# Performance work log

Measured on AMD Instinct MI355X. Metric: run time of the kernel, lower is better.

## Reference

```python
import jax, jax.numpy as jnp
import numpy as np

HEADS, POINTS = 8, 4
EPS = 1e-5
BS, C, H, W = 2, 256, 200, 200


def _layernorm(x, g, b):
    m = x.mean(-1, keepdims=True)
    v = ((x - m) ** 2).mean(-1, keepdims=True)
    return (x - m) / jnp.sqrt(v + EPS) * g + b


def _sine_pos(bs, Hh, Ww, num_feats, temperature=10000.0):
    # mmdet SinePositionalEncoding with all-zeros mask: cumsum of ones -> 1..H / 1..W
    y = jnp.arange(1, Hh + 1, dtype=jnp.float32)
    x = jnp.arange(1, Ww + 1, dtype=jnp.float32)
    dim_t = jnp.arange(num_feats, dtype=jnp.float32)
    dim_t = temperature ** (2.0 * jnp.floor(dim_t / 2.0) / num_feats)

    def interleave(p):  # p: [N, num_feats] -> [sin(p0),cos(p1),sin(p2),...]
        return jnp.stack((jnp.sin(p[:, 0::2]), jnp.cos(p[:, 1::2])), axis=-1).reshape(p.shape[0], -1)

    pos_x = interleave(x[:, None] / dim_t)  # [W, nf]
    pos_y = interleave(y[:, None] / dim_t)  # [H, nf]
    pos = jnp.concatenate([
        jnp.broadcast_to(pos_y[:, None, :], (Hh, Ww, num_feats)),
        jnp.broadcast_to(pos_x[None, :, :], (Hh, Ww, num_feats)),
    ], axis=-1)  # [H, W, 2*nf] (channel order matches cat((pos_y,pos_x),dim=1) after flatten/permute)
    return jnp.broadcast_to(pos.reshape(1, Hh * Ww, 2 * num_feats), (bs, Hh * Ww, 2 * num_feats))


def _bilinear_sample(v, x, y):
    # v: [bs, heads, H, W, hd]; x, y: [bs, heads, N] pixel coords (align_corners=False, zero padding)
    bs, nh, Hh, Ww, hd = v.shape
    vf = v.reshape(bs, nh, Hh * Ww, hd)
    x0 = jnp.floor(x)
    y0 = jnp.floor(y)
    wx = x - x0
    wy = y - y0

    def gather(xi, yi):
        valid = (xi >= 0) & (xi < Ww) & (yi >= 0) & (yi < Hh)
        xc = jnp.clip(xi, 0, Ww - 1).astype(jnp.int32)
        yc = jnp.clip(yi, 0, Hh - 1).astype(jnp.int32)
        idx = yc * Ww + xc
        g = jnp.take_along_axis(vf, idx[..., None], axis=2)  # [bs, nh, N, hd]
        return g * valid[..., None].astype(v.dtype)

    out = gather(x0, y0) * ((1 - wx) * (1 - wy))[..., None]
    out = out + gather(x0 + 1, y0) * (wx * (1 - wy))[..., None]
    out = out + gather(x0, y0 + 1) * ((1 - wx) * wy)[..., None]
    out = out + gather(x0 + 1, y0 + 1) * (wx * wy)[..., None]
    return out


def _dfa_layer(out, ref, pos, Hh, Ww, p):
    bs, Lq, Cc = out.shape
    hd = Cc // HEADS
    q = out + pos
    value = out @ p['vp_w'].T + p['vp_b']  # [bs, Lq, C]
    off = (q @ p['off_w'].T + p['off_b']).reshape(bs, Lq, HEADS, POINTS, 2)
    aw = jax.nn.softmax((q @ p['aw_w'].T + p['aw_b']).reshape(bs, Lq, HEADS, POINTS), axis=-1)
    norm = jnp.array([Ww, Hh], dtype=out.dtype)
    loc = ref[None, :, None, None, :] + off / norm  # [bs, Lq, heads, P, 2] normalized [0,1]
    x = loc[..., 0] * Ww - 0.5
    y = loc[..., 1] * Hh - 0.5
    v = value.reshape(bs, Lq, HEADS, hd).transpose(0, 2, 1, 3).reshape(bs, HEADS, Hh, Ww, hd)
    xt = x.transpose(0, 2, 1, 3).reshape(bs, HEADS, Lq * POINTS)
    yt = y.transpose(0, 2, 1, 3).reshape(bs, HEADS, Lq * POINTS)
    samp = _bilinear_sample(v, xt, yt).reshape(bs, HEADS, Lq, POINTS, hd)
    attn = jnp.einsum('bhqpd,bqhp->bqhd', samp, aw).reshape(bs, Lq, Cc)
    attn = attn @ p['op_w'].T + p['op_b']
    out = _layernorm(out + attn, p['ln1_g'], p['ln1_b'])
    ffn = jax.nn.relu(out @ p['l1_w'].T + p['l1_b']) @ p['l2_w'].T + p['l2_b']
    return _layernorm(out + ffn, p['ln2_g'], p['ln2_b'])


def setup_inputs() -> dict:
    key = jax.random.key(0)
    ks = jax.random.split(key, 20)
    s = 0.02
    L = 3
    return {
        'bev_feat': jax.random.normal(ks[0], (BS, C, H, W), jnp.float32),
        'proj_q_w': jax.random.normal(ks[1], (C, C), jnp.float32) * s,
        'proj_q_b': jax.random.normal(ks[2], (C,), jnp.float32) * s,
        'off_w': jax.random.normal(ks[3], (L, HEADS * POINTS * 2, C), jnp.float32) * s,
        'off_b': jax.random.normal(ks[4], (L, HEADS * POINTS * 2), jnp.float32) * s,
        'aw_w': jax.random.normal(ks[5], (L, HEADS * POINTS, C), jnp.float32) * s,
        'aw_b': jax.random.normal(ks[6], (L, HEADS * POINTS), jnp.float32) * s,
        'vp_w': jax.random.normal(ks[7], (L, C, C), jnp.float32) * s,
        'vp_b': jax.random.normal(ks[8], (L, C), jnp.float32) * s,
        'op_w': jax.random.normal(ks[9], (L, C, C), jnp.float32) * s,
        'op_b': jax.random.normal(ks[10], (L, C), jnp.float32) * s,
        'ln1_g': jnp.ones((L, C), jnp.float32),
        'ln1_b': jnp.zeros((L, C), jnp.float32),
        'l1_w': jax.random.normal(ks[11], (L, C, C), jnp.float32) * s,
        'l1_b': jax.random.normal(ks[12], (L, C), jnp.float32) * s,
        'l2_w': jax.random.normal(ks[13], (L, C, C), jnp.float32) * s,
        'l2_b': jax.random.normal(ks[14], (L, C), jnp.float32) * s,
        'ln2_g': jnp.ones((L, C), jnp.float32),
        'ln2_b': jnp.zeros((L, C), jnp.float32),
    }


def reference(bev_feat, proj_q_w, proj_q_b, off_w, off_b, aw_w, aw_b, vp_w, vp_b,
              op_w, op_b, ln1_g, ln1_b, l1_w, l1_b, l2_w, l2_b, ln2_g, ln2_b):
    bs, Cc, Hh, Ww = bev_feat.shape
    x = bev_feat.reshape(bs, Cc, Hh * Ww).transpose(0, 2, 1)  # [bs, HW, C]
    out = x @ proj_q_w.T + proj_q_b
    # reference points: pixel centers normalized to [0,1]
    ry, rx = jnp.meshgrid(jnp.linspace(0.5, Hh - 0.5, Hh) / Hh,
                          jnp.linspace(0.5, Ww - 0.5, Ww) / Ww, indexing='ij')
    ref = jnp.stack([rx.reshape(-1), ry.reshape(-1)], axis=-1).astype(bev_feat.dtype)  # [HW, 2]
    pos = _sine_pos(bs, Hh, Ww, Cc // 2).astype(bev_feat.dtype)
    n_layers = off_w.shape[0]
    for i in range(n_layers):
        p = dict(off_w=off_w[i], off_b=off_b[i], aw_w=aw_w[i], aw_b=aw_b[i],
                 vp_w=vp_w[i], vp_b=vp_b[i], op_w=op_w[i], op_b=op_b[i],
                 ln1_g=ln1_g[i], ln1_b=ln1_b[i], l1_w=l1_w[i], l1_b=l1_b[i],
                 l2_w=l2_w[i], l2_b=l2_b[i], ln2_g=ln2_g[i], ln2_b=ln2_b[i])
        out = _dfa_layer(out, ref, pos, Hh, Ww, p)
    return out.transpose(0, 2, 1).reshape(bs, Cc, Hh, Ww)
```

## Files before the change

kernel.cpp:

```cpp
#include <hip/hip_runtime.h>
#include <math.h>

#define HEADS 8
#define POINTS 4
#define BSZ 2
#define CDIM 256
#define HH 200
#define WW 200
#define LQ (HH * WW)
#define MTOT (BSZ * LQ)
#define NLAYERS 3
#define MPAD 40064

typedef __attribute__((ext_vector_type(8))) short shortx8;
typedef __attribute__((ext_vector_type(4))) float floatx4;

__device__ __forceinline__ ushort f2b(float f) {
    union { float f; unsigned u; } v; v.f = f;
    unsigned r = v.u + 0x7fffu + ((v.u >> 16) & 1u);
    return (ushort)(r >> 16);
}
__device__ __forceinline__ float b2f(ushort b) {
    union { unsigned u; float f; } v; v.u = ((unsigned)b) << 16;
    return v.f;
}
__device__ __forceinline__ float bitsf(unsigned u) {
    union { unsigned u; float f; } v; v.u = u;
    return v.f;
}
__device__ __forceinline__ uint packbf(float lo, float hi) {
    return (uint)f2b(lo) | ((uint)f2b(hi) << 16);
}

__device__ __forceinline__ int permc(int c) {
    return (c & ~63) | (((c & 15) << 2) | ((c & 63) >> 4));
}
__device__ __forceinline__ int iperm(int p) {
    return (p & ~63) | (((p & 3) << 4) | ((p & 63) >> 2));
}

__global__ __launch_bounds__(256)
void cvt_kernel(const float* __restrict__ in, ushort* __restrict__ out)
{
    const int i = (blockIdx.x * 256 + threadIdx.x) * 4;
    const float4 v = *(const float4*)(in + i);
    ushort4 o;
    o.x = f2b(v.x); o.y = f2b(v.y); o.z = f2b(v.z); o.w = f2b(v.w);
    *(ushort4*)(out + i) = o;
}

__global__ __launch_bounds__(256)
void cvt_perm_kernel(const float* __restrict__ in, ushort* __restrict__ out)
{
    const int idx = (blockIdx.x * 256 + threadIdx.x) * 4;
    const int rowb = idx & ~255;
    const int p0 = idx & 255;
    ushort4 o;
    o.x = f2b(in[rowb + iperm(p0 + 0)]);
    o.y = f2b(in[rowb + iperm(p0 + 1)]);
    o.z = f2b(in[rowb + iperm(p0 + 2)]);
    o.w = f2b(in[rowb + iperm(p0 + 3)]);
    *(ushort4*)(out + idx) = o;
}

__global__ __launch_bounds__(256)
void build_offaw(const float* __restrict__ offw, const float* __restrict__ offb,
                 const float* __restrict__ aww, const float* __restrict__ awb,
                 ushort* __restrict__ wout, float* __restrict__ bout)
{
    const int blk = blockIdx.x;
    const int i = blk >> 7;
    const int r = blk & 127;
    const int c = threadIdx.x;
    float v = 0.f;
    if (r < 64)      v = offw[((size_t)i * 64 + r) * CDIM + c];
    else if (r < 96) v = aww[((size_t)i * 32 + (r - 64)) * CDIM + c];
    wout[((size_t)i * 128 + r) * CDIM + permc(c)] = f2b(v);
    if (c == 0) {
        float bb = 0.f;
        if (r < 64)      bb = offb[i * 64 + r];
        else if (r < 96) bb = awb[i * 32 + (r - 64)];
        bout[i * 128 + r] = bb;
    }
}

__global__ __launch_bounds__(256)
void pos_kernel(ushort* __restrict__ pos)
{
    const int idx = blockIdx.x * 256 + threadIdx.x;
    const int c = idx & 255;
    const int l = idx >> 8;
    const int cc = c & 127;
    const float coord = (c < 128) ? (float)(l / WW + 1) : (float)(l % WW + 1);
    const float expo = (float)(2 * (cc >> 1)) * (1.0f / 128.0f);
    const float t = powf(10000.0f, expo);
    const float ph = coord / t;
    pos[(size_t)l * CDIM + permc(c)] = f2b((cc & 1) ? cosf(ph) : sinf(ph));
}

__global__ __launch_bounds__(256)
void bevT_kernel(const float* __restrict__ in, ushort* __restrict__ out)
{
    __shared__ float tile[32][33];
    const int b = blockIdx.z;
    const int l0 = blockIdx.x * 32;
    const int c0 = blockIdx.y * 32;
    const float* ib = in + (size_t)b * CDIM * LQ;
    ushort* ob = out + (size_t)b * LQ * CDIM;
    #pragma unroll
    for (int j = 0; j < 32; j += 8)
        tile[threadIdx.y + j][threadIdx.x] =
            ib[(size_t)(c0 + threadIdx.y + j) * LQ + l0 + threadIdx.x];
    __syncthreads();
    #pragma unroll
    for (int j = 0; j < 32; j += 8)
        ob[(size_t)(l0 + threadIdx.y + j) * CDIM + c0 + threadIdx.x] =
            f2b(tile[threadIdx.x][threadIdx.y + j]);
}

#define LSTR 40

template<bool RELU, bool F32OUT, bool BF16OUT, bool ROWADD>
__global__ __launch_bounds__(256)
void mfma_gemm(const ushort* __restrict__ A, const ushort* __restrict__ B,
               const float* __restrict__ bias,
               float* __restrict__ Cf, ushort* __restrict__ Cb,
               const ushort* __restrict__ rowtab,
               int N, int K)
{
    __shared__ ushort As[128 * LSTR];
    __shared__ ushort Bs[128 * LSTR];
    const int tid = threadIdx.x;
    const int lane = tid & 63;
    const int wave = tid >> 6;
    const int wr = (wave >> 1) * 64;
    const int wc = (wave & 1) * 64;
    const int rowBase = blockIdx.y * 128;
    const int colBase = blockIdx.x * 128;

    floatx4 acc[4][4];
    #pragma unroll
    for (int i = 0; i < 4; i++)
        #pragma unroll
        for (int j = 0; j < 4; j++) {
            floatx4 z = {0.f, 0.f, 0.f, 0.f};
            acc[i][j] = z;
        }

    const int strow = tid >> 2;
    const int stcol = (tid & 3) * 8;
    const int kq = (lane >> 4) * 8;
    const int lr = lane & 15;

    for (int k0 = 0; k0 < K; k0 += 32) {
        #pragma unroll
        for (int j = 0; j < 2; j++) {
            const int r = j * 64 + strow;
            const uint4 av = *(const uint4*)(A + (size_t)(rowBase + r) * K + k0 + stcol);
            const uint4 bv = *(const uint4*)(B + (size_t)(colBase + r) * K + k0 + stcol);
            *(uint4*)(As + r * LSTR + stcol) = av;
            *(uint4*)(Bs + r * LSTR + stcol) = bv;
        }
        __syncthreads();
        shortx8 af[4], bfr[4];
        #pragma unroll
        for (int t = 0; t < 4; t++) {
            af[t]  = *(const shortx8*)(As + (wr + t * 16 + lr) * LSTR + kq);
            bfr[t] = *(const shortx8*)(Bs + (wc + t * 16 + lr) * LSTR + kq);
        }
        #pragma unroll
        for (int mt = 0; mt < 4; mt++)
            #pragma unroll
            for (int nt = 0; nt < 4; nt++)
                acc[mt][nt] = __builtin_amdgcn_mfma_f32_16x16x32_bf16(
                    af[mt], bfr[nt], acc[mt][nt], 0, 0, 0);
        __syncthreads();
    }

    const int colB = colBase + wc + lr;
    const int rowB = rowBase + wr + (lane >> 4) * 4;
    #pragma unroll
    for (int mt = 0; mt < 4; mt++) {
        #pragma unroll
        for (int r = 0; r < 4; r++) {
            const int m = rowB + mt * 16 + r;
            const int pr = (m >= LQ) ? m - LQ : m;
            #pragma unroll
            for (int nt = 0; nt < 4; nt++) {
                const int n = colB + nt * 16;
                float v = acc[mt][nt][r];
                if (ROWADD) v += b2f(rowtab[(size_t)pr * 384 + n]);
                else        v += bias[n];
                if (RELU) v = fmaxf(v, 0.f);
                if (F32OUT) Cf[(size_t)m * N + n] = v;
                if (BF16OUT) Cb[(size_t)m * N + n] = f2b(v);
            }
        }
    }
}

template<bool RELU, bool LN, bool F32OUT, bool BF16OUT, bool PERMC>
__global__ __launch_bounds__(512, 1)
void gemm_fused(const ushort* __restrict__ A, const ushort* __restrict__ B,
                const float* __restrict__ bias,
                float* __restrict__ resid, ushort* __restrict__ Cb,
                const float* __restrict__ g, const float* __restrict__ beta)
{
    __shared__ ushort As[2][128 * LSTR];
    __shared__ ushort Bs[2][256 * LSTR];

    const int tid = threadIdx.x;
    const int lane = tid & 63;
    const int wave = tid >> 6;
    const int lr = lane & 15;
    const int hi = lane >> 4;
    const int rowBase = blockIdx.x * 128;
    const int wr = (wave >> 2) * 64;
    const int wc = (wave & 3) * 64;

    floatx4 acc[4][4];
    #pragma unroll
    for (int i = 0; i < 4; i++)
        #pragma unroll
        for (int j = 0; j < 4; j++) {
            floatx4 z = {0.f, 0.f, 0.f, 0.f};
            acc[i][j] = z;
        }

    const int strow = tid >> 2;
    const int stcol = (tid & 3) * 8;
    const int kq = hi * 8;

    const ushort* ag = A + (size_t)(rowBase + strow) * CDIM + stcol;
    const ushort* bg = B + (size_t)strow * CDIM + stcol;

    {
        const uint4 av  = *(const uint4*)(ag);
        const uint4 bv0 = *(const uint4*)(bg);
        const uint4 bv1 = *(const uint4*)(bg + 128 * CDIM);
        *(uint4*)(As[0] + strow * LSTR + stcol) = av;
        *(uint4*)(Bs[0] + strow * LSTR + stcol) = bv0;
        *(uint4*)(Bs[0] + (strow + 128) * LSTR + stcol) = bv1;
    }

    #pragma unroll
    for (int kt = 0; kt < 8; ++kt) {
        const int p = kt & 1;
        __syncthreads();
        uint4 av, bv0, bv1;
        if (kt < 7) {
            const int ko = (kt + 1) * 32;
            av  = *(const uint4*)(ag + ko);
            bv0 = *(const uint4*)(bg + ko);
            bv1 = *(const uint4*)(bg + ko + 128 * CDIM);
        }
        shortx8 af[4], bfr[4];
        #pragma unroll
        for (int t = 0; t < 4; t++) {
            af[t]  = *(const shortx8*)(As[p] + (wr + t * 16 + lr) * LSTR + kq);
            bfr[t] = *(const shortx8*)(Bs[p] + (wc + t * 16 + lr) * LSTR + kq);
        }
        #pragma unroll
        for (int mt = 0; mt < 4; mt++)
            #pragma unroll
            for (int nt = 0; nt < 4; nt++)
                acc[mt][nt] = __builtin_amdgcn_mfma_f32_16x16x32_bf16(
                    af[mt], bfr[nt], acc[mt][nt], 0, 0, 0);
        if (kt < 7) {
            *(uint4*)(As[p ^ 1] + strow * LSTR + stcol) = av;
            *(uint4*)(Bs[p ^ 1] + strow * LSTR + stcol) = bv0;
            *(uint4*)(Bs[p ^ 1] + (strow + 128) * LSTR + stcol) = bv1;
        }
    }
    __syncthreads();

    float bcol[4];
    #pragma unroll
    for (int nt = 0; nt < 4; nt++) bcol[nt] = bias[wc + nt * 16 + lr];

    if (LN) {
        float2 (*red)[4] = (float2(*)[4])As[0];
        #pragma unroll
        for (int mt = 0; mt < 4; mt++) {
            #pragma unroll
            for (int r = 0; r < 4; r++) {
                const int mrel = wr + mt * 16 + hi * 4 + r;
                const int m = rowBase + mrel;
                const float4 rv = *(const float4*)(resid + (size_t)m * CDIM + wc + lr * 4);
                float s = 0.f, sq = 0.f;
                #pragma unroll
                for (int nt = 0; nt < 4; nt++) {
                    float x = acc[mt][nt][r] + bcol[nt] + (&rv.x)[nt];
                    acc[mt][nt][r] = x;
                    s += x; sq += x * x;
                }
                #pragma unroll
                for (int o = 8; o >= 1; o >>= 1) {
                    s  += __shfl_xor(s, o, 64);
                    sq += __shfl_xor(sq, o, 64);
                }
                if (lr == 0) { float2 t2; t2.x = s; t2.y = sq; red[mrel][wave & 3] = t2; }
            }
        }
        __syncthreads();
        float gcol[4], btcol[4];
        #pragma unroll
        for (int nt = 0; nt < 4; nt++) {
            gcol[nt]  = g[wc + nt * 16 + lr];
            btcol[nt] = beta[wc + nt * 16 + lr];
        }
        #pragma unroll
        for (int mt = 0; mt < 4; mt++) {
            #pragma unroll
            for (int r = 0; r < 4; r++) {
                const int mrel = wr + mt * 16 + hi * 4 + r;
                const int m = rowBase + mrel;
                const float2 t0 = red[mrel][0], t1 = red[mrel][1];
                const float2 t2 = red[mrel][2], t3 = red[mrel][3];
                const float S  = (t0.x + t1.x) + (t2.x + t3.x);
                const float SQ = (t0.y + t1.y) + (t2.y + t3.y);
                const float mean = S * (1.0f / CDIM);
                const float var = SQ * (1.0f / CDIM) - mean * mean;
                const float rstd = rsqrtf(var + 1e-5f);
                float4 wv;
                ushort4 ob;
                #pragma unroll
                for (int nt = 0; nt < 4; nt++) {
                    const float y = (acc[mt][nt][r] - mean) * rstd * gcol[nt] + btcol[nt];
                    (&wv.x)[nt] = y;
                    if (BF16OUT) (&ob.x)[nt] = f2b(y);
                }
                *(float4*)(resid + (size_t)m * CDIM + wc + lr * 4) = wv;
                if (BF16OUT) *(ushort4*)(Cb + (size_t)m * CDIM + wc + lr * 4) = ob;
            }
        }
    } else {
        #pragma unroll
        for (int mt = 0; mt < 4; mt++) {
            #pragma unroll
            for (int r = 0; r < 4; r++) {
                const int m = rowBase + wr + mt * 16 + hi * 4 + r;
                float4 wv;
                ushort4 ob;
                #pragma unroll
                for (int nt = 0; nt < 4; nt++) {
                    float y = acc[mt][nt][r] + bcol[nt];
                    if (RELU) y = fmaxf(y, 0.f);
                    (&wv.x)[nt] = y;
                    if (PERMC) {
                        if (BF16OUT) (&ob.x)[nt] = f2b(y);
                    } else {
                        const int col = wc + nt * 16 + lr;
                        if (BF16OUT) Cb[(size_t)m * CDIM + col] = f2b(y);
                    }
                }
                if (F32OUT) *(float4*)(resid + (size_t)m * CDIM + wc + lr * 4) = wv;
                if (PERMC && BF16OUT)
                    *(ushort4*)(Cb + (size_t)m * CDIM + wc + lr * 4) = ob;
            }
        }
    }
}

__global__ __launch_bounds__(256)
void sample_kernel(const ushort* __restrict__ val,
                   const float* __restrict__ offaw,
                   ushort* __restrict__ attn)
{
    const int tid = threadIdx.x;
    const int m = blockIdx.x * 8 + (tid >> 5);
    const int lane = tid & 31;
    const int head = lane >> 2;
    const int c = head * 32 + (lane & 3) * 8;
    const int b = (m >= LQ) ? 1 : 0;
    const int l = m - (b ? LQ : 0);

    const float* row = offaw + (size_t)m * 128;
    const float4 lg  = *(const float4*)(row + 64 + head * 4);
    const float4 o01 = *(const float4*)(row + head * 8);
    const float4 o23 = *(const float4*)(row + head * 8 + 4);

    const float mx = fmaxf(fmaxf(lg.x, lg.y), fmaxf(lg.z, lg.w));
    const float e0 = expf(lg.x - mx), e1 = expf(lg.y - mx);
    const float e2 = expf(lg.z - mx), e3 = expf(lg.w - mx);
    const float inv = 1.0f / (e0 + e1 + e2 + e3);
    const float awv[4] = {e0 * inv, e1 * inv, e2 * inv, e3 * inv};

    const float lx = (float)(l % WW);
    const float ly = (float)(l / WW);
    const float px[4] = {lx + o01.x, lx + o01.z, lx + o23.x, lx + o23.z};
    const float py[4] = {ly + o01.y, ly + o01.w, ly + o23.y, ly + o23.w};

    const ushort* vb = val + (size_t)b * LQ * CDIM;
    uint4 cv[16];
    float cw[16];
    #pragma unroll
    for (int p = 0; p < POINTS; p++) {
        const float x = px[p], y = py[p];
        const float xf = floorf(x), yf = floorf(y);
        const int x0 = (int)xf, y0 = (int)yf;
        const float wx = x - xf, wy = y - yf;
        const int x0c = min(max(x0, 0), WW - 1);
        const int x1c = min(max(x0 + 1, 0), WW - 1);
        const int y0c = min(max(y0, 0), HH - 1);
        const int y1c = min(max(y0 + 1, 0), HH - 1);
        const float vx0 = (x0 >= 0 && x0 < WW) ? 1.f : 0.f;
        const float vx1 = (x0 + 1 >= 0 && x0 + 1 < WW) ? 1.f : 0.f;
        const float vy0 = (y0 >= 0 && y0 < HH) ? 1.f : 0.f;
        const float vy1 = (y0 + 1 >= 0 && y0 + 1 < HH) ? 1.f : 0.f;
        const float a = awv[p];
        cw[p * 4 + 0] = a * (1.f - wx) * (1.f - wy) * vx0 * vy0;
        cw[p * 4 + 1] = a * wx * (1.f - wy) * vx1 * vy0;
        cw[p * 4 + 2] = a * (1.f - wx) * wy * vx0 * vy1;
        cw[p * 4 + 3] = a * wx * wy * vx1 * vy1;
        const int r0 = y0c * WW, r1 = y1c * WW;
        cv[p * 4 + 0] = *(const uint4*)(vb + (((unsigned)(r0 + x0c)) << 8) + c);
        cv[p * 4 + 1] = *(const uint4*)(vb + (((unsigned)(r0 + x1c)) << 8) + c);
        cv[p * 4 + 2] = *(const uint4*)(vb + (((unsigned)(r1 + x0c)) << 8) + c);
        cv[p * 4 + 3] = *(const uint4*)(vb + (((unsigned)(r1 + x1c)) << 8) + c);
    }
    float a0 = 0.f, a1 = 0.f, a2 = 0.f, a3 = 0.f;
    float a4 = 0.f, a5 = 0.f, a6 = 0.f, a7 = 0.f;
    #pragma unroll
    for (int i = 0; i < 16; i++) {
        const float wgt = cw[i];
        a0 = fmaf(wgt, bitsf(cv[i].x << 16), a0);
        a1 = fmaf(wgt, bitsf(cv[i].x & 0xffff0000u), a1);
        a2 = fmaf(wgt, bitsf(cv[i].y << 16), a2);
        a3 = fmaf(wgt, bitsf(cv[i].y & 0xffff0000u), a3);
        a4 = fmaf(wgt, bitsf(cv[i].z << 16), a4);
        a5 = fmaf(wgt, bitsf(cv[i].z & 0xffff0000u), a5);
        a6 = fmaf(wgt, bitsf(cv[i].w << 16), a6);
        a7 = fmaf(wgt, bitsf(cv[i].w & 0xffff0000u), a7);
    }
    uint4 o;
    o.x = packbf(a0, a1); o.y = packbf(a2, a3);
    o.z = packbf(a4, a5); o.w = packbf(a6, a7);
    *(uint4*)(attn + (size_t)m * CDIM + c) = o;
}

__global__ __launch_bounds__(256)
void transpose_out(const float* __restrict__ in, float* __restrict__ outp)
{
    __shared__ float tile[32][33];
    const int b = blockIdx.z;
    const int l0 = blockIdx.x * 32;
    const int c0 = blockIdx.y * 32;
    const float* ib = in + (size_t)b * LQ * CDIM;
    float* ob = outp + (size_t)b * CDIM * LQ;
    #pragma unroll
    for (int j = 0; j < 32; j += 8)
        tile[threadIdx.y + j][threadIdx.x] =
            ib[(size_t)(l0 + threadIdx.y + j) * CDIM + c0 + threadIdx.x];
    __syncthreads();
    #pragma unroll
    for (int j = 0; j < 32; j += 8)
        ob[(size_t)iperm(c0 + threadIdx.y + j) * LQ + l0 + threadIdx.x] =
            tile[threadIdx.x][threadIdx.y + j];
}

extern "C" void kernel_launch(void* const* d_in, const int* in_sizes, int n_in,
                              void* d_out, int out_size, void* d_ws, size_t ws_size,
                              hipStream_t stream)
{
    const float* bev      = (const float*)d_in[0];
    const float* proj_q_w = (const float*)d_in[1];
    const float* proj_q_b = (const float*)d_in[2];
    const float* off_w    = (const float*)d_in[3];
    const float* off_b    = (const float*)d_in[4];
    const float* aw_w     = (const float*)d_in[5];
    const float* aw_b     = (const float*)d_in[6];
    const float* vp_w     = (const float*)d_in[7];
    const float* vp_b     = (const float*)d_in[8];
    const float* op_w     = (const float*)d_in[9];
    const float* op_b     = (const float*)d_in[10];
    const float* ln1_g    = (const float*)d_in[11];
    const float* ln1_b    = (const float*)d_in[12];
    const float* l1_w     = (const float*)d_in[13];
    const float* l1_b     = (const float*)d_in[14];
    const float* l2_w     = (const float*)d_in[15];
    const float* l2_b     = (const float*)d_in[16];
    const float* ln2_g    = (const float*)d_in[17];
    const float* ln2_b    = (const float*)d_in[18];
    float* outp = (float*)d_out;

    char* w = (char*)d_ws;
    float*  out_f    = (float*)(w);
    float*  offaw_f  = (float*)(w + 81920000);
    ushort* attn_b   = (ushort*)(w + 122880000);
    ushort* out_b    = (ushort*)(w + 163840000);
    ushort* posoff_b = (ushort*)(w + 204800000);
    ushort* val_b    = (ushort*)(w + 245760000);
    ushort* pos_b    = (ushort*)(w + 286720000);
    ushort* w_b      = (ushort*)(w + 307200000);
    ushort* wproj = w_b;
    ushort* wvp   = w_b + 65536;
    ushort* wop   = w_b + 65536 + 196608;
    ushort* wl1   = w_b + 65536 + 2 * 196608;
    ushort* wl2   = w_b + 65536 + 3 * 196608;
    ushort* wofa  = w_b + 65536 + 4 * 196608;
    float*  bofa  = (float*)(w + 307200000 + 2 * (65536 + 4 * 196608 + 98304));

    const dim3 blk(256);
    const dim3 blk512(512);

    cvt_kernel<<<dim3(65536 / 1024), blk, 0, stream>>>(proj_q_w, wproj);
    cvt_perm_kernel<<<dim3(196608 / 1024), blk, 0, stream>>>(vp_w, wvp);
    cvt_kernel<<<dim3(196608 / 1024), blk, 0, stream>>>(op_w, wop);
    cvt_perm_kernel<<<dim3(196608 / 1024), blk, 0, stream>>>(l1_w, wl1);
    cvt_perm_kernel<<<dim3(196608 / 1024), blk, 0, stream>>>(l2_w, wl2);
    build_offaw<<<dim3(3 * 128), blk, 0, stream>>>(off_w, off_b, aw_w, aw_b, wofa, bofa);
    pos_kernel<<<dim3((LQ * CDIM) / 256), blk, 0, stream>>>(pos_b);
    bevT_kernel<<<dim3(LQ / 32, CDIM / 32, BSZ), dim3(32, 8), 0, stream>>>(bev, val_b);

    mfma_gemm<false, false, true, false><<<dim3(3, MPAD / 128), blk, 0, stream>>>(
        pos_b, wofa, bofa, nullptr, posoff_b, nullptr, 384, CDIM);

    const dim3 gF(MTOT / 128);
    const dim3 g128(1, MTOT / 128);

    gemm_fused<false, false, true, true, true><<<gF, blk512, 0, stream>>>(
        val_b, wproj, proj_q_b, out_f, out_b, nullptr, nullptr);

    for (int i = 0; i < NLAYERS; i++) {
        gemm_fused<false, false, false, true, false><<<gF, blk512, 0, stream>>>(
            out_b, wvp + (size_t)i * 65536, vp_b + (size_t)i * CDIM,
            nullptr, val_b, nullptr, nullptr);
        mfma_gemm<false, true, false, true><<<g128, blk, 0, stream>>>(
            out_b, wofa + (size_t)i * 32768, nullptr,
            offaw_f, nullptr, posoff_b + (size_t)i * 128, 128, CDIM);
        sample_kernel<<<dim3(MTOT / 8), blk, 0, stream>>>(val_b, offaw_f, attn_b);
        gemm_fused<false, true, false, true, true><<<gF, blk512, 0, stream>>>(
            attn_b, wop + (size_t)i * 65536, op_b + (size_t)i * CDIM,
            out_f, out_b,
            ln1_g + (size_t)i * CDIM, ln1_b + (size_t)i * CDIM);
        gemm_fused<true, false, false, true, true><<<gF, blk512, 0, stream>>>(
            out_b, wl1 + (size_t)i * 65536, l1_b + (size_t)i * CDIM,
            nullptr, val_b, nullptr, nullptr);
        if (i < NLAYERS - 1) {
            gemm_fused<false, true, false, true, true><<<gF, blk512, 0, stream>>>(
                val_b, wl2 + (size_t)i * 65536, l2_b + (size_t)i * CDIM,
                out_f, out_b,
                ln2_g + (size_t)i * CDIM, ln2_b + (size_t)i * CDIM);
        } else {
            gemm_fused<false, true, false, false, true><<<gF, blk512, 0, stream>>>(
                val_b, wl2 + (size_t)i * 65536, l2_b + (size_t)i * CDIM,
                out_f, nullptr,
                ln2_g + (size_t)i * CDIM, ln2_b + (size_t)i * CDIM);
        }
    }

    transpose_out<<<dim3(LQ / 32, CDIM / 32, BSZ), dim3(32, 8), 0, stream>>>(out_f, outp);
}
```

Measured before the change: 1.044 ms.

## Fuse output projection, LN1, FFN and LN2 into one kernel per layer

Replaces three separate GEMM launches per layer (output projection with LN1, FFN linear1 with ReLU, FFN linear2 with LN2) with a single kernel. The LN1 result and the hidden activation stay in LDS as bf16, and the LN1 fp32 residual is kept in registers. This is meant to remove global round trips of the intermediate activations, the reload of the fp32 residual, and launch overhead. In exchange the kernel uses more LDS, holds two accumulator sets (higher register pressure), and adds serialized phases within each block.

```diff
diff --git a/kernel.cpp b/kernel.cpp
--- a/kernel.cpp
+++ b/kernel.cpp
@@ -199,12 +199,11 @@
     }
 }
 
-template<bool RELU, bool LN, bool F32OUT, bool BF16OUT, bool PERMC>
+template<bool RELU, bool F32OUT, bool BF16OUT, bool PERMC>
 __global__ __launch_bounds__(512, 1)
 void gemm_fused(const ushort* __restrict__ A, const ushort* __restrict__ B,
                 const float* __restrict__ bias,
-                float* __restrict__ resid, ushort* __restrict__ Cb,
-                const float* __restrict__ g, const float* __restrict__ beta)
+                float* __restrict__ resid, ushort* __restrict__ Cb)
 {
     __shared__ ushort As[2][128 * LSTR];
     __shared__ ushort Bs[2][256 * LSTR];
@@ -272,13 +271,122 @@
             *(uint4*)(Bs[p ^ 1] + (strow + 128) * LSTR + stcol) = bv1;
         }
     }
-    __syncthreads();
 
     float bcol[4];
     #pragma unroll
     for (int nt = 0; nt < 4; nt++) bcol[nt] = bias[wc + nt * 16 + lr];
 
-    if (LN) {
+    #pragma unroll
+    for (int mt = 0; mt < 4; mt++) {
+        #pragma unroll
+        for (int r = 0; r < 4; r++) {
+            const int m = rowBase + wr + mt * 16 + hi * 4 + r;
+            float4 wv;
+            ushort4 ob;
+            #pragma unroll
+            for (int nt = 0; nt < 4; nt++) {
+                float y = acc[mt][nt][r] + bcol[nt];
+                if (RELU) y = fmaxf(y, 0.f);
+                (&wv.x)[nt] = y;
+                if (PERMC) {
+                    if (BF16OUT) (&ob.x)[nt] = f2b(y);
+                } else {
+                    const int col = wc + nt * 16 + lr;
+                    if (BF16OUT) Cb[(size_t)m * CDIM + col] = f2b(y);
+                }
+            }
+            if (F32OUT) *(float4*)(resid + (size_t)m * CDIM + wc + lr * 4) = wv;
+            if (PERMC && BF16OUT)
+                *(ushort4*)(Cb + (size_t)m * CDIM + wc + lr * 4) = ob;
+        }
+    }
+}
+
+#define LSTR3 264
+
+template<bool BF16OUT>
+__global__ __launch_bounds__(512, 1)
+void ffn_fused(const ushort* __restrict__ attn, const ushort* __restrict__ Wop,
+               const float* __restrict__ opb,
+               const ushort* __restrict__ Wl1, const float* __restrict__ l1b,
+               const ushort* __restrict__ Wl2, const float* __restrict__ l2b,
+               float* __restrict__ resid, ushort* __restrict__ outb,
+               const float* __restrict__ g1, const float* __restrict__ b1,
+               const float* __restrict__ g2, const float* __restrict__ b2)
+{
+    __shared__ ushort As[2][128 * LSTR];
+    __shared__ ushort Bs[2][256 * LSTR];
+    __shared__ ushort Ls[128 * LSTR3];
+
+    const int tid = threadIdx.x;
+    const int lane = tid & 63;
+    const int wave = tid >> 6;
+    const int lr = lane & 15;
+    const int hi = lane >> 4;
+    const int rowBase = blockIdx.x * 128;
+    const int wr = (wave >> 2) * 64;
+    const int wc = (wave & 3) * 64;
+
+    const int strow = tid >> 2;
+    const int stcol = (tid & 3) * 8;
+    const int kq = hi * 8;
+
+    floatx4 acc1[4][4];
+    #pragma unroll
+    for (int i = 0; i < 4; i++)
+        #pragma unroll
+        for (int j = 0; j < 4; j++) {
+            floatx4 z = {0.f, 0.f, 0.f, 0.f};
+            acc1[i][j] = z;
+        }
+
+    {
+        const ushort* ag = attn + (size_t)(rowBase + strow) * CDIM + stcol;
+        const ushort* bg = Wop + (size_t)strow * CDIM + stcol;
+        {
+            const uint4 av  = *(const uint4*)(ag);
+            const uint4 bv0 = *(const uint4*)(bg);
+            const uint4 bv1 = *(const uint4*)(bg + 128 * CDIM);
+            *(uint4*)(As[0] + strow * LSTR + stcol) = av;
+            *(uint4*)(Bs[0] + strow * LSTR + stcol) = bv0;
+            *(uint4*)(Bs[0] + (strow + 128) * LSTR + stcol) = bv1;
+        }
+        #pragma unroll
+        for (int kt = 0; kt < 8; ++kt) {
+            const int p = kt & 1;
+            __syncthreads();
+            uint4 av, bv0, bv1;
+            if (kt < 7) {
+                const int ko = (kt + 1) * 32;
+                av  = *(const uint4*)(ag + ko);
+                bv0 = *(const uint4*)(bg + ko);
+                bv1 = *(const uint4*)(bg + ko + 128 * CDIM);
+            }
+            shortx8 af[4], bfr[4];
+            #pragma unroll
+            for (int t = 0; t < 4; t++) {
+                af[t]  = *(const shortx8*)(As[p] + (wr + t * 16 + lr) * LSTR + kq);
+                bfr[t] = *(const shortx8*)(Bs[p] + (wc + t * 16 + lr) * LSTR + kq);
+            }
+            #pragma unroll
+            for (int mt = 0; mt < 4; mt++)
+                #pragma unroll
+                for (int nt = 0; nt < 4; nt++)
+                    acc1[mt][nt] = __builtin_amdgcn_mfma_f32_16x16x32_bf16(
+                        af[mt], bfr[nt], acc1[mt][nt], 0, 0, 0);
+            if (kt < 7) {
+                *(uint4*)(As[p ^ 1] + strow * LSTR + stcol) = av;
+                *(uint4*)(Bs[p ^ 1] + strow * LSTR + stcol) = bv0;
+                *(uint4*)(Bs[p ^ 1] + (strow + 128) * LSTR + stcol) = bv1;
+            }
+        }
+        __syncthreads();
+    }
+
+    {
+        float bcol[4];
+        #pragma unroll
+        for (int nt = 0; nt < 4; nt++) bcol[nt] = opb[wc + nt * 16 + lr];
         float2 (*red)[4] = (float2(*)[4])As[0];
         #pragma unroll
         for (int mt = 0; mt < 4; mt++) {
@@ -290,8 +398,8 @@
                 float s = 0.f, sq = 0.f;
                 #pragma unroll
                 for (int nt = 0; nt < 4; nt++) {
-                    float x = acc[mt][nt][r] + bcol[nt] + (&rv.x)[nt];
-                    acc[mt][nt][r] = x;
+                    float x = acc1[mt][nt][r] + bcol[nt] + (&rv.x)[nt];
+                    acc1[mt][nt][r] = x;
                     s += x; sq += x * x;
                 }
                 #pragma unroll
@@ -306,8 +414,169 @@
         float gcol[4], btcol[4];
         #pragma unroll
         for (int nt = 0; nt < 4; nt++) {
-            gcol[nt]  = g[wc + nt * 16 + lr];
-            btcol[nt] = beta[wc + nt * 16 + lr];
+            gcol[nt]  = g1[wc + nt * 16 + lr];
+            btcol[nt] = b1[wc + nt * 16 + lr];
+        }
+        #pragma unroll
+        for (int mt = 0; mt < 4; mt++) {
+            #pragma unroll
+            for (int r = 0; r < 4; r++) {
+                const int mrel = wr + mt * 16 + hi * 4 + r;
+                const float2 t0 = red[mrel][0], t1 = red[mrel][1];
+                const float2 t2 = red[mrel][2], t3 = red[mrel][3];
+                const float S  = (t0.x + t1.x) + (t2.x + t3.x);
+                const float SQ = (t0.y + t1.y) + (t2.y + t3.y);
+                const float mean = S * (1.0f / CDIM);
+                const float var = SQ * (1.0f / CDIM) - mean * mean;
+                const float rstd = rsqrtf(var + 1e-5f);
+                ushort4 yb;
+                #pragma unroll
+                for (int nt = 0; nt < 4; nt++) {
+                    const float y = (acc1[mt][nt][r] - mean) * rstd * gcol[nt] + btcol[nt];
+                    acc1[mt][nt][r] = y;
+                    (&yb.x)[nt] = f2b(y);
+                }
+                *(ushort4*)(Ls + mrel * LSTR3 + wc + lr * 4) = yb;
+            }
+        }
+    }
+
+    floatx4 acc2[4][4];
+    #pragma unroll
+    for (int i = 0; i < 4; i++)
+        #pragma unroll
+        for (int j = 0; j < 4; j++) {
+            floatx4 z = {0.f, 0.f, 0.f, 0.f};
+            acc2[i][j] = z;
+        }
+    {
+        const ushort* bg = Wl1 + (size_t)strow * CDIM + stcol;
+        {
+            const uint4 bv0 = *(const uint4*)(bg);
+            const uint4 bv1 = *(const uint4*)(bg + 128 * CDIM);
+            *(uint4*)(Bs[0] + strow * LSTR + stcol) = bv0;
+            *(uint4*)(Bs[0] + (strow + 128) * LSTR + stcol) = bv1;
+        }
+        #pragma unroll
+        for (int kt = 0; kt < 8; ++kt) {
+            const int p = kt & 1;
+            __syncthreads();
+            uint4 bv0, bv1;
+            if (kt < 7) {
+                const int ko = (kt + 1) * 32;
+                bv0 = *(const uint4*)(bg + ko);
+                bv1 = *(const uint4*)(bg + ko + 128 * CDIM);
+            }
+            shortx8 af[4], bfr[4];
+            #pragma unroll
+            for (int t = 0; t < 4; t++) {
+                af[t]  = *(const shortx8*)(Ls + (wr + t * 16 + lr) * LSTR3 + kt * 32 + kq);
+                bfr[t] = *(const shortx8*)(Bs[p] + (wc + t * 16 + lr) * LSTR + kq);
+            }
+            #pragma unroll
+            for (int mt = 0; mt < 4; mt++)
+                #pragma unroll
+                for (int nt = 0; nt < 4; nt++)
+                    acc2[mt][nt] = __builtin_amdgcn_mfma_f32_16x16x32_bf16(
+                        af[mt], bfr[nt], acc2[mt][nt], 0, 0, 0);
+            if (kt < 7) {
+                *(uint4*)(Bs[p ^ 1] + strow * LSTR + stcol) = bv0;
+                *(uint4*)(Bs[p ^ 1] + (strow + 128) * LSTR + stcol) = bv1;
+            }
+        }
+        __syncthreads();
+        float bcol2[4];
+        #pragma unroll
+        for (int nt = 0; nt < 4; nt++) bcol2[nt] = l1b[wc + nt * 16 + lr];
+        #pragma unroll
+        for (int mt = 0; mt < 4; mt++) {
+            #pragma unroll
+            for (int r = 0; r < 4; r++) {
+                const int mrel = wr + mt * 16 + hi * 4 + r;
+                ushort4 hb;
+                #pragma unroll
+                for (int nt = 0; nt < 4; nt++)
+                    (&hb.x)[nt] = f2b(fmaxf(acc2[mt][nt][r] + bcol2[nt], 0.f));
+                *(ushort4*)(Ls + mrel * LSTR3 + wc + lr * 4) = hb;
+            }
+        }
+    }
+
+    #pragma unroll
+    for (int i = 0; i < 4; i++)
+        #pragma unroll
+        for (int j = 0; j < 4; j++) {
+            floatx4 z = {0.f, 0.f, 0.f, 0.f};
+            acc2[i][j] = z;
+        }
+    {
+        const ushort* bg = Wl2 + (size_t)strow * CDIM + stcol;
+        {
+            const uint4 bv0 = *(const uint4*)(bg);
+            const uint4 bv1 = *(const uint4*)(bg + 128 * CDIM);
+            *(uint4*)(Bs[0] + strow * LSTR + stcol) = bv0;
+            *(uint4*)(Bs[0] + (strow + 128) * LSTR + stcol) = bv1;
+        }
+        #pragma unroll
+        for (int kt = 0; kt < 8; ++kt) {
+            const int p = kt & 1;
+            __syncthreads();
+            uint4 bv0, bv1;
+            if (kt < 7) {
+                const int ko = (kt + 1) * 32;
+                bv0 = *(const uint4*)(bg + ko);
+                bv1 = *(const uint4*)(bg + ko + 128 * CDIM);
+            }
+            shortx8 af[4], bfr[4];
+            #pragma unroll
+            for (int t = 0; t < 4; t++) {
+                af[t]  = *(const shortx8*)(Ls + (wr + t * 16 + lr) * LSTR3 + kt * 32 + kq);
+                bfr[t] = *(const shortx8*)(Bs[p] + (wc + t * 16 + lr) * LSTR + kq);
+            }
+            #pragma unroll
+            for (int mt = 0; mt < 4; mt++)
+                #pragma unroll
+                for (int nt = 0; nt < 4; nt++)
+                    acc2[mt][nt] = __builtin_amdgcn_mfma_f32_16x16x32_bf16(
+                        af[mt], bfr[nt], acc2[mt][nt], 0, 0, 0);
+            if (kt < 7) {
+                *(uint4*)(Bs[p ^ 1] + strow * LSTR + stcol) = bv0;
+                *(uint4*)(Bs[p ^ 1] + (strow + 128) * LSTR + stcol) = bv1;
+            }
+        }
+        __syncthreads();
+    }
+    {
+        float bcol3[4];
+        #pragma unroll
+        for (int nt = 0; nt < 4; nt++) bcol3[nt] = l2b[wc + nt * 16 + lr];
+        float2 (*red)[4] = (float2(*)[4])As[0];
+        #pragma unroll
+        for (int mt = 0; mt < 4; mt++) {
+            #pragma unroll
+            for (int r = 0; r < 4; r++) {
+                const int mrel = wr + mt * 16 + hi * 4 + r;
+                float s = 0.f, sq = 0.f;
+                #pragma unroll
+                for (int nt = 0; nt < 4; nt++) {
+                    float x = acc2[mt][nt][r] + bcol3[nt] + acc1[mt][nt][r];
+                    acc2[mt][nt][r] = x;
+                    s += x; sq += x * x;
+                }
+                #pragma unroll
+                for (int o = 8; o >= 1; o >>= 1) {
+                    s  += __shfl_xor(s, o, 64);
+                    sq += __shfl_xor(sq, o, 64);
+                }
+                if (lr == 0) { float2 t2; t2.x = s; t2.y = sq; red[mrel][wave & 3] = t2; }
+            }
+        }
+        __syncthreads();
+        float gcol[4], btcol[4];
+        #pragma unroll
+        for (int nt = 0; nt < 4; nt++) {
+            gcol[nt]  = g2[wc + nt * 16 + lr];
+            btcol[nt] = b2[wc + nt * 16 + lr];
         }
         #pragma unroll
         for (int mt = 0; mt < 4; mt++) {
@@ -326,37 +595,12 @@
                 ushort4 ob;
                 #pragma unroll
                 for (int nt = 0; nt < 4; nt++) {
-                    const float y = (acc[mt][nt][r] - mean) * rstd * gcol[nt] + btcol[nt];
+                    const float y = (acc2[mt][nt][r] - mean) * rstd * gcol[nt] + btcol[nt];
                     (&wv.x)[nt] = y;
                     if (BF16OUT) (&ob.x)[nt] = f2b(y);
                 }
                 *(float4*)(resid + (size_t)m * CDIM + wc + lr * 4) = wv;
-                if (BF16OUT) *(ushort4*)(Cb + (size_t)m * CDIM + wc + lr * 4) = ob;
-            }
-        }
-    } else {
-        #pragma unroll
-        for (int mt = 0; mt < 4; mt++) {
-            #pragma unroll
-            for (int r = 0; r < 4; r++) {
-                const int m = rowBase + wr + mt * 16 + hi * 4 + r;
-                float4 wv;
-                ushort4 ob;
-                #pragma unroll
-                for (int nt = 0; nt < 4; nt++) {
-                    float y = acc[mt][nt][r] + bcol[nt];
-                    if (RELU) y = fmaxf(y, 0.f);
-                    (&wv.x)[nt] = y;
-                    if (PERMC) {
-                        if (BF16OUT) (&ob.x)[nt] = f2b(y);
-                    } else {
-                        const int col = wc + nt * 16 + lr;
-                        if (BF16OUT) Cb[(size_t)m * CDIM + col] = f2b(y);
-                    }
-                }
-                if (F32OUT) *(float4*)(resid + (size_t)m * CDIM + wc + lr * 4) = wv;
-                if (PERMC && BF16OUT)
-                    *(ushort4*)(Cb + (size_t)m * CDIM + wc + lr * 4) = ob;
+                if (BF16OUT) *(ushort4*)(outb + (size_t)m * CDIM + wc + lr * 4) = ob;
             }
         }
     }
@@ -519,33 +763,32 @@
     const dim3 gF(MTOT / 128);
     const dim3 g128(1, MTOT / 128);
 
-    gemm_fused<false, false, true, true, true><<<gF, blk512, 0, stream>>>(
-        val_b, wproj, proj_q_b, out_f, out_b, nullptr, nullptr);
+    gemm_fused<false, true, true, true><<<gF, blk512, 0, stream>>>(
+        val_b, wproj, proj_q_b, out_f, out_b);
 
     for (int i = 0; i < NLAYERS; i++) {
-        gemm_fused<false, false, false, true, false><<<gF, blk512, 0, stream>>>(
+        gemm_fused<false, false, true, false><<<gF, blk512, 0, stream>>>(
             out_b, wvp + (size_t)i * 65536, vp_b + (size_t)i * CDIM,
-            nullptr, val_b, nullptr, nullptr);
+            nullptr, val_b);
         mfma_gemm<false, true, false, true><<<g128, blk, 0, stream>>>(
             out_b, wofa + (size_t)i * 32768, nullptr,
             offaw_f, nullptr, posoff_b + (size_t)i * 128, 128, CDIM);
         sample_kernel<<<dim3(MTOT / 8), blk, 0, stream>>>(val_b, offaw_f, attn_b);
-        gemm_fused<false, true, false, true, true><<<gF, blk512, 0, stream>>>(
-            attn_b, wop + (size_t)i * 65536, op_b + (size_t)i * CDIM,
-            out_f, out_b,
-            ln1_g + (size_t)i * CDIM, ln1_b + (size_t)i * CDIM);
-        gemm_fused<true, false, false, true, true><<<gF, blk512, 0, stream>>>(
-            out_b, wl1 + (size_t)i * 65536, l1_b + (size_t)i * CDIM,
-            nullptr, val_b, nullptr, nullptr);
         if (i < NLAYERS - 1) {
-            gemm_fused<false, true, false, true, true><<<gF, blk512, 0, stream>>>(
-                val_b, wl2 + (size_t)i * 65536, l2_b + (size_t)i * CDIM,
+            ffn_fused<true><<<gF, blk512, 0, stream>>>(
+                attn_b, wop + (size_t)i * 65536, op_b + (size_t)i * CDIM,
+                wl1 + (size_t)i * 65536, l1_b + (size_t)i * CDIM,
+                wl2 + (size_t)i * 65536, l2_b + (size_t)i * CDIM,
                 out_f, out_b,
+                ln1_g + (size_t)i * CDIM, ln1_b + (size_t)i * CDIM,
                 ln2_g + (size_t)i * CDIM, ln2_b + (size_t)i * CDIM);
         } else {
-            gemm_fused<false, true, false, false, true><<<gF, blk512, 0, stream>>>(
-                val_b, wl2 + (size_t)i * 65536, l2_b + (size_t)i * CDIM,
+            ffn_fused<false><<<gF, blk512, 0, stream>>>(
+                attn_b, wop + (size_t)i * 65536, op_b + (size_t)i * CDIM,
+                wl1 + (size_t)i * 65536, l1_b + (size_t)i * CDIM,
+                wl2 + (size_t)i * 65536, l2_b + (size_t)i * CDIM,
                 out_f, nullptr,
+                ln1_g + (size_t)i * CDIM, ln1_b + (size_t)i * CDIM,
                 ln2_g + (size_t)i * CDIM, ln2_b + (size_t)i * CDIM);
         }
     }
```

New measurement: 942.6 us. 9.7% less time.
